# Kernel tuning notes

Measured on AMD Instinct MI355X. Metric: run time of the kernel, lower is better.

## Reference

```python
import jax, jax.numpy as jnp
import numpy as np

H, W = 496, 432  # ny, nx
C = 64           # pillar_dim == hidden_dim == NUM_BEV_FEATURES
B, N = 2, 8192   # batch size, non-empty pillars per batch
EPS = 1e-5


def _ln(x, g, b):
    m = jnp.mean(x, axis=-1, keepdims=True)
    v = jnp.var(x, axis=-1, keepdims=True)
    return (x - m) * jax.lax.rsqrt(v + EPS) * g + b


def _apply_rope(x):
    # x: [H, W, C] -> 2D RoPE-rotated features, matching torch reference math
    half = C // 2
    theta = 10000.0 ** (-(jnp.arange(half, dtype=jnp.float32) / half))
    h = jnp.linspace(-1.0, 1.0, H)
    w = jnp.linspace(-1.0, 1.0, W)
    hs = jnp.sin(h[:, None, None] * theta)  # [H,1,half]
    hc = jnp.cos(h[:, None, None] * theta)
    ws = jnp.sin(w[None, :, None] * theta)  # [1,W,half]
    wc = jnp.cos(w[None, :, None] * theta)
    x1, x2 = x[..., :half], x[..., half:]
    return jnp.concatenate(
        [x1 * hc * wc - x2 * hs * ws, x1 * hs * ws + x2 * hc * wc], axis=-1)


def setup_inputs() -> dict:
    key = jax.random.key(0)
    ks = jax.random.split(key, 8)
    rng = np.random.default_rng(0)
    # sorted UNIQUE flat indices per batch (boolean-mask gather order == sorted index order)
    idx = np.stack([np.sort(rng.choice(H * W, size=N, replace=False)) for _ in range(B)])
    s = 0.05
    return {
        "pillar_features": jax.random.normal(ks[0], (B, N, C), jnp.float32),
        "voxel_indices": jnp.asarray(idx, jnp.int32),
        "q_w": jax.random.normal(ks[1], (C, C), jnp.float32) * s,
        "q_b": jnp.zeros((C,), jnp.float32),
        "k_w": jax.random.normal(ks[2], (C, C), jnp.float32) * s,
        "k_b": jnp.zeros((C,), jnp.float32),
        "v_w": jax.random.normal(ks[3], (C, C), jnp.float32) * s,
        "v_b": jnp.zeros((C,), jnp.float32),
        "ffn_w1": jax.random.normal(ks[4], (C, C), jnp.float32) * s,
        "ffn_b1": jnp.zeros((C,), jnp.float32),
        "ffn_w2": jax.random.normal(ks[5], (C, C), jnp.float32) * s,
        "ffn_b2": jnp.zeros((C,), jnp.float32),
        "n1_g": jnp.ones((C,), jnp.float32),
        "n1_b": jnp.zeros((C,), jnp.float32),
        "n2_g": jnp.ones((C,), jnp.float32),
        "n2_b": jnp.zeros((C,), jnp.float32),
    }


def reference(pillar_features, voxel_indices, q_w, q_b, k_w, k_b, v_w, v_b,
              ffn_w1, ffn_b1, ffn_w2, ffn_b2, n1_g, n1_b, n2_g, n2_b):
    def per_batch(pillars, idx):
        # scatter pillars to dense BEV grid [H*W, C]
        dense = jnp.zeros((H * W, C), pillars.dtype).at[idx].set(pillars)
        x = dense.reshape(H, W, C)
        x = x + _apply_rope(x)                  # residual RoPE add
        flat = x.reshape(H * W, C)
        g = flat[idx]                           # masked gather (sorted index order)
        gn = _ln(g, n1_g, n1_b)
        Q = gn @ q_w.T + q_b                    # [N, C]
        K = gn @ k_w.T + k_b
        V = gn @ v_w.T + v_b
        attn = jax.nn.softmax(Q @ K.T, axis=-1)  # [N, N] full attention
        att = attn @ V + g
        h1 = jax.nn.gelu(_ln(att, n2_g, n2_b) @ ffn_w1.T + ffn_b1, approximate=False)
        upd = h1 @ ffn_w2.T + ffn_b2 + att
        out = flat.at[idx].set(upd)             # scatter back
        return out.T.reshape(C, H, W)
    return jax.vmap(per_batch)(pillar_features, voxel_indices)  # [B, C, H, W]
```

## Files before the change

### kernel.cpp

```cpp
#include <hip/hip_runtime.h>
#include <hip/hip_bf16.h>
#include <math.h>

#define HH 496
#define WW 432
#define CC 64
#define BB 2
#define NN 8192
#define HW_ (HH * WW)
#define SPLIT 8
#define KVPS (NN / SPLIT)
#define LOG2E 1.44269504088896f
#define DEFER_THR 11.541560327f

#if __has_builtin(__builtin_amdgcn_exp2f)
#define EXP2(x) __builtin_amdgcn_exp2f(x)
#else
#define EXP2(x) exp2f(x)
#endif

typedef __attribute__((ext_vector_type(8))) short bhalf8;
typedef __attribute__((ext_vector_type(4))) float f32x4;

__device__ __forceinline__ unsigned short f2bf(float f) {
  union { float f; unsigned int u; } v; v.f = f;
  unsigned int r = (v.u + 0x7fffu + ((v.u >> 16) & 1u)) >> 16;
  return (unsigned short)r;
}

__device__ __forceinline__ float bf2f(unsigned short u) {
  union { unsigned int u; float f; } v;
  v.u = ((unsigned int)u) << 16;
  return v.f;
}

__device__ __forceinline__ void gload16(const void* g, void* l) {
  __builtin_amdgcn_global_load_lds(
      (const __attribute__((address_space(1))) void*)g,
      (__attribute__((address_space(3))) void*)l, 16, 0, 0);
}

__global__ void prep_kernel(float* __restrict__ tabHS, float* __restrict__ tabHC,
                            float* __restrict__ tabWS, float* __restrict__ tabWC,
                            int* __restrict__ map) {
  int tid = blockIdx.x * blockDim.x + threadIdx.x;
  const int ntab = (HH + WW) * 32;
  if (tid < ntab) {
    int j = tid & 31;
    float theta = __expf(-(float)j * (9.210340371976184f / 32.f));
    if (tid < HH * 32) {
      int i = tid >> 5;
      float h = -1.f + 2.f * (float)i / (float)(HH - 1);
      float a = h * theta;
      tabHS[tid] = sinf(a);
      tabHC[tid] = cosf(a);
    } else {
      int t2 = tid - HH * 32;
      int i = t2 >> 5;
      float w = -1.f + 2.f * (float)i / (float)(WW - 1);
      float a = w * theta;
      tabWS[t2] = sinf(a);
      tabWC[t2] = cosf(a);
    }
  } else if (tid < ntab + BB * HW_) {
    map[tid - ntab] = -1;
  }
}

__global__ __launch_bounds__(256) void qkv_kernel(
    const float* __restrict__ pillar, const int* __restrict__ vidx,
    const float* __restrict__ tabHS, const float* __restrict__ tabHC,
    const float* __restrict__ tabWS, const float* __restrict__ tabWC,
    const float* __restrict__ qw, const float* __restrict__ kw,
    const float* __restrict__ vw,
    const float* __restrict__ qb, const float* __restrict__ kbias,
    const float* __restrict__ vb,
    const float* __restrict__ n1g, const float* __restrict__ n1b,
    float* __restrict__ g_out, unsigned short* __restrict__ Qb,
    unsigned short* __restrict__ Kb, unsigned short* __restrict__ Vt,
    int* __restrict__ map) {
  __shared__ unsigned short Aln[32][72];
  __shared__ unsigned short Wq[64][72], Wk[64][72], Wv[64][72];
  __shared__ unsigned int Vbo[64][20];
  int tid = threadIdx.x, wid = tid >> 6, lane = tid & 63;
  int l16 = lane & 15, lg = lane >> 4;
  int pt0 = blockIdx.x * 32;
  int b = pt0 >> 13, n0 = pt0 & (NN - 1);

  {
    int c = tid >> 2, k0 = (tid & 3) * 16;
#pragma unroll
    for (int mmm = 0; mmm < 3; mmm++) {
      const float* src = (mmm == 0 ? qw : mmm == 1 ? kw : vw) + c * 64 + k0;
      unsigned int pk[8];
#pragma unroll
      for (int j = 0; j < 8; j++) {
        float lo = src[2 * j], hi = src[2 * j + 1];
        asm("v_cvt_pk_bf16_f32 %0, %1, %2" : "=v"(pk[j]) : "v"(lo), "v"(hi));
      }
      unsigned short(*Wm)[72] = mmm == 0 ? Wq : mmm == 1 ? Wk : Wv;
      unsigned int* dst = (unsigned int*)&Wm[c][k0];
      *(uint4*)dst = make_uint4(pk[0], pk[1], pk[2], pk[3]);
      *(uint4*)(dst + 4) = make_uint4(pk[4], pk[5], pk[6], pk[7]);
    }
  }

  float n1g_l = n1g[lane], n1b_l = n1b[lane];
#pragma unroll 4
  for (int i = 0; i < 8; i++) {
    int p = wid * 8 + i;
    int pt = pt0 + p;
    float x = pillar[(size_t)pt * CC + lane];
    int pos = vidx[pt];
    int h = pos / WW, w = pos - h * WW;
    int j = lane & 31;
    float x1 = __shfl(x, j), x2 = __shfl(x, j + 32);
    float hs = tabHS[h * 32 + j], hc = tabHC[h * 32 + j];
    float ws = tabWS[w * 32 + j], wc = tabWC[w * 32 + j];
    float rope = (lane < 32) ? (x1 * hc * wc - x2 * hs * ws)
                             : (x1 * hs * ws + x2 * hc * wc);
    float gv = x + rope;
    g_out[(size_t)pt * CC + lane] = gv;
    float s = gv;
    for (int mm2 = 1; mm2 <= 32; mm2 <<= 1) s += __shfl_xor(s, mm2);
    float mean = s * (1.f / 64.f);
    float d = gv - mean;
    float vsum = d * d;
    for (int mm2 = 1; mm2 <= 32; mm2 <<= 1) vsum += __shfl_xor(vsum, mm2);
    float rstd = rsqrtf(vsum * (1.f / 64.f) + 1e-5f);
    float gn = d * rstd * n1g_l + n1b_l;
    Aln[p][lane] = f2bf(gn);
    if (lane == 0) map[b * HW_ + pos] = pt & (NN - 1);
  }
  __syncthreads();

#pragma unroll
  for (int j = 0; j < 6; j++) {
    int job = wid * 6 + j;
    int t = job / 12;
    int rem = job % 12;
    int mat = rem >> 2;
    int ct = rem & 3;
    bhalf8 aG0 = *(bhalf8*)&Aln[t * 16 + l16][lg * 8];
    bhalf8 aG1 = *(bhalf8*)&Aln[t * 16 + l16][32 + lg * 8];
    unsigned short(*Wm)[72] = mat == 0 ? Wq : mat == 1 ? Wk : Wv;
    bhalf8 bw0 = *(bhalf8*)&Wm[ct * 16 + l16][lg * 8];
    bhalf8 bw1 = *(bhalf8*)&Wm[ct * 16 + l16][32 + lg * 8];
    const float* bptr = mat == 0 ? qb : mat == 1 ? kbias : vb;
    float bias = bptr[ct * 16 + l16];
    f32x4 d = (f32x4){0.f, 0.f, 0.f, 0.f};
    d = __builtin_amdgcn_mfma_f32_16x16x32_bf16(aG0, bw0, d, 0, 0, 0);
    d = __builtin_amdgcn_mfma_f32_16x16x32_bf16(aG1, bw1, d, 0, 0, 0);
    if (mat == 0) {
#pragma unroll
      for (int r = 0; r < 4; r++) {
        size_t gi = (size_t)(pt0 + t * 16 + 4 * lg + r) * CC + ct * 16 + l16;
        Qb[gi] = f2bf((d[r] + bias) * LOG2E);
      }
    } else if (mat == 1) {
#pragma unroll
      for (int r = 0; r < 4; r++) {
        size_t gi = (size_t)(pt0 + t * 16 + 4 * lg + r) * CC + ct * 16 + l16;
        Kb[gi] = f2bf(d[r] + bias);
      }
    } else {
      float e0 = d[0] + bias, e1 = d[1] + bias;
      float e2 = d[2] + bias, e3 = d[3] + bias;
      unsigned int v0, v1;
      asm("v_cvt_pk_bf16_f32 %0, %1, %2" : "=v"(v0) : "v"(e0), "v"(e1));
      asm("v_cvt_pk_bf16_f32 %0, %1, %2" : "=v"(v1) : "v"(e2), "v"(e3));
      Vbo[ct * 16 + l16][t * 8 + 2 * lg + 0] = v0;
      Vbo[ct * 16 + l16][t * 8 + 2 * lg + 1] = v1;
    }
  }
  __syncthreads();
  {
    int c = tid >> 2, ch = tid & 3;
    uint4 w0 = *(uint4*)&Vbo[c][ch * 4];
    *(uint4*)(Vt + ((size_t)b * CC + c) * NN + n0 + ch * 8) = w0;
  }
}

__global__ __attribute__((amdgpu_flat_work_group_size(512, 512),
                          amdgpu_waves_per_eu(4, 4))) void attn_kernel(
    const unsigned short* __restrict__ Qb, const unsigned short* __restrict__ Kb,
    const unsigned short* __restrict__ Vt,
    unsigned short* __restrict__ OPb, float* __restrict__ Mb,
    float* __restrict__ Lb) {
  __shared__ unsigned short Kt[2][64 * 64];
  __shared__ unsigned short Vl[2][64 * 64];
  __shared__ unsigned short Plds[8][32][72];
  int tidx = threadIdx.x;
  int wid = tidx >> 6, lane = tidx & 63;
  int l16 = lane & 15, lg = lane >> 4;
  int blk = blockIdx.x;
  int s = blk & (SPLIT - 1);
  int tb = blk >> 3;
  int b = tb >> 5;
  int tile = tb & 31;
  int q0 = tile * 256 + wid * 32;
  int kvbeg = s * KVPS;
  const unsigned short* Q = Qb + (size_t)b * NN * CC;
  const unsigned short* K = Kb + (size_t)b * NN * CC;
  const unsigned short* V = Vt + (size_t)b * CC * NN;

  bhalf8 bQ0 = *(const bhalf8*)(Q + (size_t)(q0 + l16) * CC + lg * 8);
  bhalf8 bQ1 = *(const bhalf8*)(Q + (size_t)(q0 + l16) * CC + 32 + lg * 8);
  bhalf8 bQ2 = *(const bhalf8*)(Q + (size_t)(q0 + 16 + l16) * CC + lg * 8);
  bhalf8 bQ3 = *(const bhalf8*)(Q + (size_t)(q0 + 16 + l16) * CC + 32 + lg * 8);

  int r8 = lane >> 3, chn = lane & 7;
  int sch = chn ^ r8;
  const unsigned short* Ksrc = K + (size_t)(8 * wid + r8) * CC + sch * 8;
  const unsigned short* Vsrc = V + (size_t)(8 * wid + r8) * NN + sch * 8;
  unsigned short* KtW = &Kt[0][0] + (8 * wid) * 64;
  unsigned short* VlW = &Vl[0][0] + (8 * wid) * 64;

  f32x4 acc0[4], acc1[4];
#pragma unroll
  for (int i = 0; i < 4; i++) {
    acc0[i] = (f32x4){0.f, 0.f, 0.f, 0.f};
    acc1[i] = (f32x4){0.f, 0.f, 0.f, 0.f};
  }
  float m = -1e30f, Lp0 = 0.f, Lp1 = 0.f;
  int sw8 = (l16 & 7) * 8;

  auto stage = [&](int bufi, int kv0) {
    gload16(Ksrc + (size_t)kv0 * CC, KtW + bufi * 4096);
    gload16(Vsrc + kv0, VlW + bufi * 4096);
  };

  auto body = [&](int buf, int kv0) {
    const unsigned short* Kb_ = &Kt[buf][0];
    const unsigned short* Vb_ = &Vl[buf][0];
    f32x4 St[4], Su[4];
    __builtin_amdgcn_s_setprio(1);
#pragma unroll
    for (int t = 0; t < 4; t++) {
      const unsigned short* kr = Kb_ + (16 * t + l16) * 64;
      bhalf8 aK0 = *(const bhalf8*)(kr + ((lg * 8) ^ sw8));
      bhalf8 aK1 = *(const bhalf8*)(kr + (((lg + 4) * 8) ^ sw8));
      f32x4 sa = (f32x4){0.f, 0.f, 0.f, 0.f};
      f32x4 sb = (f32x4){0.f, 0.f, 0.f, 0.f};
      sa = __builtin_amdgcn_mfma_f32_16x16x32_bf16(aK0, bQ0, sa, 0, 0, 0);
      sa = __builtin_amdgcn_mfma_f32_16x16x32_bf16(aK1, bQ1, sa, 0, 0, 0);
      sb = __builtin_amdgcn_mfma_f32_16x16x32_bf16(aK0, bQ2, sb, 0, 0, 0);
      sb = __builtin_amdgcn_mfma_f32_16x16x32_bf16(aK1, bQ3, sb, 0, 0, 0);
      St[t] = sa;
      Su[t] = sb;
    }
    __builtin_amdgcn_s_setprio(0);
    float m0a = fmaxf(fmaxf(St[0][0], St[0][1]), fmaxf(St[0][2], St[0][3]));
    float m0b = fmaxf(fmaxf(St[1][0], St[1][1]), fmaxf(St[1][2], St[1][3]));
    float m0c = fmaxf(fmaxf(St[2][0], St[2][1]), fmaxf(St[2][2], St[2][3]));
    float m0d = fmaxf(fmaxf(St[3][0], St[3][1]), fmaxf(St[3][2], St[3][3]));
    float m1a = fmaxf(fmaxf(Su[0][0], Su[0][1]), fmaxf(Su[0][2], Su[0][3]));
    float m1b = fmaxf(fmaxf(Su[1][0], Su[1][1]), fmaxf(Su[1][2], Su[1][3]));
    float m1c = fmaxf(fmaxf(Su[2][0], Su[2][1]), fmaxf(Su[2][2], Su[2][3]));
    float m1d = fmaxf(fmaxf(Su[3][0], Su[3][1]), fmaxf(Su[3][2], Su[3][3]));
    float pm = fmaxf(fmaxf(fmaxf(m0a, m0b), fmaxf(m0c, m0d)),
                     fmaxf(fmaxf(m1a, m1b), fmaxf(m1c, m1d)));
    pm = fmaxf(pm, __shfl_xor(pm, 16));
    pm = fmaxf(pm, __shfl_xor(pm, 32));
    if (!__all(pm <= m + DEFER_THR)) {
      float mn = fmaxf(m, pm);
      float sc = EXP2(m - mn);
      m = mn;
      float scq[4];
#pragma unroll
      for (int r = 0; r < 4; r++) scq[r] = __shfl(sc, 4 * lg + r);
#pragma unroll
      for (int cg = 0; cg < 4; cg++)
#pragma unroll
        for (int r = 0; r < 4; r++) {
          acc0[cg][r] *= scq[r];
          acc1[cg][r] *= scq[r];
        }
      Lp0 *= sc;
      Lp1 *= sc;
    }
#pragma unroll
    for (int t = 0; t < 4; t++)
#pragma unroll
      for (int r = 0; r < 4; r++) {
        float p0 = EXP2(St[t][r] - m);
        float p1 = EXP2(Su[t][r] - m);
        St[t][r] = p0; Su[t][r] = p1;
        Lp0 += p0; Lp1 += p1;
      }
#pragma unroll
    for (int t = 0; t < 4; t++) {
      unsigned int pw0, pw1, pw2, pw3;
      float a0 = St[t][0], a1 = St[t][1], a2 = St[t][2], a3 = St[t][3];
      float b0 = Su[t][0], b1 = Su[t][1], b2 = Su[t][2], b3 = Su[t][3];
      asm("v_cvt_pk_bf16_f32 %0, %1, %2" : "=v"(pw0) : "v"(a0), "v"(a1));
      asm("v_cvt_pk_bf16_f32 %0, %1, %2" : "=v"(pw1) : "v"(a2), "v"(a3));
      asm("v_cvt_pk_bf16_f32 %0, %1, %2" : "=v"(pw2) : "v"(b0), "v"(b1));
      asm("v_cvt_pk_bf16_f32 %0, %1, %2" : "=v"(pw3) : "v"(b2), "v"(b3));
      *(uint2*)&Plds[wid][l16][16 * t + 4 * lg] = make_uint2(pw0, pw1);
      *(uint2*)&Plds[wid][16 + l16][16 * t + 4 * lg] = make_uint2(pw2, pw3);
    }
#pragma unroll
    for (int ch = 0; ch < 2; ch++) {
      bhalf8 aP0 = *(bhalf8*)&Plds[wid][l16][ch * 32 + lg * 8];
      bhalf8 aP1 = *(bhalf8*)&Plds[wid][16 + l16][ch * 32 + lg * 8];
      __builtin_amdgcn_s_setprio(1);
#pragma unroll
      for (int cg = 0; cg < 4; cg++) {
        bhalf8 bV = *(const bhalf8*)(Vb_ + (cg * 16 + l16) * 64 +
                                     (((4 * ch + lg) * 8) ^ sw8));
        acc0[cg] = __builtin_amdgcn_mfma_f32_16x16x32_bf16(aP0, bV, acc0[cg], 0, 0, 0);
        acc1[cg] = __builtin_amdgcn_mfma_f32_16x16x32_bf16(aP1, bV, acc1[cg], 0, 0, 0);
      }
      __builtin_amdgcn_s_setprio(0);
    }
  };

  stage(0, kvbeg);
  __syncthreads();
  const int nstep = KVPS / 64;
  for (int stp = 0; stp < nstep; stp += 2) {
    int kv0 = kvbeg + stp * 64;
    if (stp + 1 < nstep) stage(1, kv0 + 64);
    body(0, kv0);
    __syncthreads();
    if (stp + 2 < nstep) stage(0, kv0 + 128);
    body(1, kv0 + 64);
    __syncthreads();
  }
  size_t rowb = ((size_t)s * BB + b) * NN;
#pragma unroll
  for (int cg = 0; cg < 4; cg++)
#pragma unroll
    for (int r = 0; r < 4; r++) {
      OPb[(rowb + q0 + 4 * lg + r) * CC + cg * 16 + l16] = f2bf(acc0[cg][r]);
      OPb[(rowb + q0 + 16 + 4 * lg + r) * CC + cg * 16 + l16] = f2bf(acc1[cg][r]);
    }
  Lp0 += __shfl_xor(Lp0, 16);
  Lp0 += __shfl_xor(Lp0, 32);
  Lp1 += __shfl_xor(Lp1, 16);
  Lp1 += __shfl_xor(Lp1, 32);
  if (lg == 0) {
    Mb[rowb + q0 + l16] = m;
    Lb[rowb + q0 + l16] = Lp0;
    Mb[rowb + q0 + 16 + l16] = m;
    Lb[rowb + q0 + 16 + l16] = Lp1;
  }
}

__global__ __launch_bounds__(256) void ffn_kernel(
    const unsigned short* __restrict__ OPb, const float* __restrict__ Mb,
    const float* __restrict__ Lb, const float* __restrict__ g_in,
    const float* __restrict__ w1, const float* __restrict__ w2,
    const float* __restrict__ b1, const float* __restrict__ b2,
    const float* __restrict__ n2g, const float* __restrict__ n2b,
    float* __restrict__ upd) {
  __shared__ unsigned short Atile[32][72];
  __shared__ unsigned short Htile[32][72];
  __shared__ float aT[32][66];
  __shared__ unsigned short W1[64][72], W2[64][72];
  int tid = threadIdx.x, wid = tid >> 6, lane = tid & 63;
  int l16 = lane & 15, lg = lane >> 4;
  int pt0 = blockIdx.x * 32;

  {
    int c = tid >> 2, k0 = (tid & 3) * 16;
#pragma unroll
    for (int mmm = 0; mmm < 2; mmm++) {
      const float* src = (mmm == 0 ? w1 : w2) + c * 64 + k0;
      unsigned int pk[8];
#pragma unroll
      for (int j = 0; j < 8; j++) {
        float lo = src[2 * j], hi = src[2 * j + 1];
        asm("v_cvt_pk_bf16_f32 %0, %1, %2" : "=v"(pk[j]) : "v"(lo), "v"(hi));
      }
      unsigned short(*Wm)[72] = mmm == 0 ? W1 : W2;
      unsigned int* dst = (unsigned int*)&Wm[c][k0];
      *(uint4*)dst = make_uint4(pk[0], pk[1], pk[2], pk[3]);
      *(uint4*)(dst + 4) = make_uint4(pk[4], pk[5], pk[6], pk[7]);
    }
  }

  float n2g_l = n2g[lane], n2b_l = n2b[lane];
#pragma unroll 2
  for (int i = 0; i < 8; i++) {
    int p = wid * 8 + i;
    int pt = pt0 + p;
    float mv[SPLIT];
    float M = -1e30f;
#pragma unroll
    for (int s = 0; s < SPLIT; s++) {
      mv[s] = Mb[s * (BB * NN) + pt];
      M = fmaxf(M, mv[s]);
    }
    float accv = 0.f, Ls = 0.f;
#pragma unroll
    for (int s = 0; s < SPLIT; s++) {
      float w = EXP2(mv[s] - M);
      accv += w * bf2f(OPb[((size_t)s * (BB * NN) + pt) * CC + lane]);
      Ls += w * Lb[s * (BB * NN) + pt];
    }
    float a = accv / Ls + g_in[(size_t)pt * CC + lane];
    aT[p][lane] = a;
    float s2 = a;
    for (int mm2 = 1; mm2 <= 32; mm2 <<= 1) s2 += __shfl_xor(s2, mm2);
    float mean = s2 * (1.f / 64.f);
    float d = a - mean;
    float vsum = d * d;
    for (int mm2 = 1; mm2 <= 32; mm2 <<= 1) vsum += __shfl_xor(vsum, mm2);
    float rstd = rsqrtf(vsum * (1.f / 64.f) + 1e-5f);
    Atile[p][lane] = f2bf(d * rstd * n2g_l + n2b_l);
  }
  __syncthreads();

#pragma unroll
  for (int j = 0; j < 2; j++) {
    int job = wid * 2 + j;
    int t = job >> 2, ct = job & 3;
    bhalf8 aH0 = *(bhalf8*)&Atile[t * 16 + l16][lg * 8];
    bhalf8 aH1 = *(bhalf8*)&Atile[t * 16 + l16][32 + lg * 8];
    bhalf8 bw0 = *(bhalf8*)&W1[ct * 16 + l16][lg * 8];
    bhalf8 bw1 = *(bhalf8*)&W1[ct * 16 + l16][32 + lg * 8];
    float b1v = b1[ct * 16 + l16];
    f32x4 d1 = (f32x4){0.f, 0.f, 0.f, 0.f};
    d1 = __builtin_amdgcn_mfma_f32_16x16x32_bf16(aH0, bw0, d1, 0, 0, 0);
    d1 = __builtin_amdgcn_mfma_f32_16x16x32_bf16(aH1, bw1, d1, 0, 0, 0);
#pragma unroll
    for (int r = 0; r < 4; r++) {
      float h = d1[r] + b1v;
      h = 0.5f * h * (1.f + erff(h * 0.70710678118654752f));
      Htile[t * 16 + 4 * lg + r][ct * 16 + l16] = f2bf(h);
    }
  }
  __syncthreads();

#pragma unroll
  for (int j = 0; j < 2; j++) {
    int job = wid * 2 + j;
    int t = job >> 2, ct = job & 3;
    bhalf8 aF0 = *(bhalf8*)&Htile[t * 16 + l16][lg * 8];
    bhalf8 aF1 = *(bhalf8*)&Htile[t * 16 + l16][32 + lg * 8];
    bhalf8 bw0 = *(bhalf8*)&W2[ct * 16 + l16][lg * 8];
    bhalf8 bw1 = *(bhalf8*)&W2[ct * 16 + l16][32 + lg * 8];
    float b2v = b2[ct * 16 + l16];
    f32x4 d2 = (f32x4){0.f, 0.f, 0.f, 0.f};
    d2 = __builtin_amdgcn_mfma_f32_16x16x32_bf16(aF0, bw0, d2, 0, 0, 0);
    d2 = __builtin_amdgcn_mfma_f32_16x16x32_bf16(aF1, bw1, d2, 0, 0, 0);
#pragma unroll
    for (int r = 0; r < 4; r++) {
      int p = t * 16 + 4 * lg + r;
      upd[(size_t)(pt0 + p) * CC + ct * 16 + l16] = d2[r] + b2v + aT[p][ct * 16 + l16];
    }
  }
}

__global__ __launch_bounds__(256) void out_kernel(
    const int* __restrict__ map, const float* __restrict__ upd,
    float* __restrict__ out) {
  int b = blockIdx.x / (HW_ / 256);
  int pos = (blockIdx.x % (HW_ / 256)) * 256 + threadIdx.x;
  int r = map[b * HW_ + pos];
  float4 vals[16];
  if (r >= 0) {
    const float4* up = (const float4*)(upd + ((size_t)b * NN + r) * CC);
#pragma unroll
    for (int i = 0; i < 16; i++) vals[i] = up[i];
  } else {
#pragma unroll
    for (int i = 0; i < 16; i++) vals[i] = make_float4(0.f, 0.f, 0.f, 0.f);
  }
  float* o = out + (size_t)b * CC * HW_ + pos;
#pragma unroll
  for (int i = 0; i < 16; i++) {
    o[(size_t)(4 * i + 0) * HW_] = vals[i].x;
    o[(size_t)(4 * i + 1) * HW_] = vals[i].y;
    o[(size_t)(4 * i + 2) * HW_] = vals[i].z;
    o[(size_t)(4 * i + 3) * HW_] = vals[i].w;
  }
}

extern "C" void kernel_launch(void* const* d_in, const int* in_sizes, int n_in,
                              void* d_out, int out_size, void* d_ws, size_t ws_size,
                              hipStream_t stream) {
  const float* pillar = (const float*)d_in[0];
  const int* vidx = (const int*)d_in[1];
  const float* qw = (const float*)d_in[2];
  const float* qb = (const float*)d_in[3];
  const float* kw = (const float*)d_in[4];
  const float* kb = (const float*)d_in[5];
  const float* vw = (const float*)d_in[6];
  const float* vb = (const float*)d_in[7];
  const float* w1 = (const float*)d_in[8];
  const float* b1 = (const float*)d_in[9];
  const float* w2 = (const float*)d_in[10];
  const float* b2 = (const float*)d_in[11];
  const float* n1g = (const float*)d_in[12];
  const float* n1b = (const float*)d_in[13];
  const float* n2g = (const float*)d_in[14];
  const float* n2b = (const float*)d_in[15];
  float* out = (float*)d_out;

  char* ws = (char*)d_ws;
  size_t off = 0;
  auto take = [&](size_t bytes) -> char* {
    off = (off + 255) & ~(size_t)255;
    char* p = ws + off;
    off += bytes;
    return p;
  };
  float* tabHS = (float*)take((size_t)HH * 32 * 4);
  float* tabHC = (float*)take((size_t)HH * 32 * 4);
  float* tabWS = (float*)take((size_t)WW * 32 * 4);
  float* tabWC = (float*)take((size_t)WW * 32 * 4);
  float* gbuf = (float*)take((size_t)BB * NN * CC * 4);
  float* updb = (float*)take((size_t)BB * NN * CC * 4);
  unsigned short* Qb = (unsigned short*)take((size_t)BB * NN * CC * 2);
  unsigned short* Kb = (unsigned short*)take((size_t)BB * NN * CC * 2);
  unsigned short* Vt = (unsigned short*)take((size_t)BB * CC * NN * 2);
  unsigned short* OPb = (unsigned short*)take((size_t)SPLIT * BB * NN * CC * 2);
  float* Mbuf = (float*)take((size_t)SPLIT * BB * NN * 4);
  float* Lbuf = (float*)take((size_t)SPLIT * BB * NN * 4);
  int* map = (int*)take((size_t)BB * HW_ * 4);

  int preptot = (HH + WW) * 32 + BB * HW_;
  prep_kernel<<<(preptot + 255) / 256, 256, 0, stream>>>(
      tabHS, tabHC, tabWS, tabWC, map);
  qkv_kernel<<<BB * NN / 32, 256, 0, stream>>>(
      pillar, vidx, tabHS, tabHC, tabWS, tabWC, qw, kw, vw, qb, kb, vb,
      n1g, n1b, gbuf, Qb, Kb, Vt, map);
  attn_kernel<<<BB * (NN / 256) * SPLIT, 512, 0, stream>>>(Qb, Kb, Vt, OPb, Mbuf, Lbuf);
  ffn_kernel<<<BB * NN / 32, 256, 0, stream>>>(OPb, Mbuf, Lbuf, gbuf, w1, w2,
                                               b1, b2, n2g, n2b, updb);
  out_kernel<<<BB * (HW_ / 256), 256, 0, stream>>>(map, updb, out);
}
```

Measured before the change: 99.39 us.

## Double KV split, process query halves sequentially to cut registers, raise occupancy

The attention kernel's KV split count goes from 8 to 16, doubling the number of blocks and halving each block's KV range. The per-step body is split into two sequential half passes, one per 16-row query group, each with its own running max. This shrinks live score registers and the P staging buffer so the occupancy hint can rise from 4 to 6 waves per EU. The cost is more partial outputs for the FFN kernel to merge, more partial-output memory traffic, and repeated K/V LDS reads across the two halves.

```diff
diff --git a/kernel.cpp b/kernel.cpp
--- a/kernel.cpp
+++ b/kernel.cpp
@@ -8,7 +8,7 @@
 #define BB 2
 #define NN 8192
 #define HW_ (HH * WW)
-#define SPLIT 8
+#define SPLIT 16
 #define KVPS (NN / SPLIT)
 #define LOG2E 1.44269504088896f
 #define DEFER_THR 11.541560327f
@@ -182,20 +182,20 @@
 }
 
 __global__ __attribute__((amdgpu_flat_work_group_size(512, 512),
-                          amdgpu_waves_per_eu(4, 4))) void attn_kernel(
+                          amdgpu_waves_per_eu(6, 6))) void attn_kernel(
     const unsigned short* __restrict__ Qb, const unsigned short* __restrict__ Kb,
     const unsigned short* __restrict__ Vt,
     unsigned short* __restrict__ OPb, float* __restrict__ Mb,
     float* __restrict__ Lb) {
   __shared__ unsigned short Kt[2][64 * 64];
   __shared__ unsigned short Vl[2][64 * 64];
-  __shared__ unsigned short Plds[8][32][72];
+  __shared__ unsigned short Plds[8][16][72];
   int tidx = threadIdx.x;
   int wid = tidx >> 6, lane = tidx & 63;
   int l16 = lane & 15, lg = lane >> 4;
   int blk = blockIdx.x;
   int s = blk & (SPLIT - 1);
-  int tb = blk >> 3;
+  int tb = blk >> 4;
   int b = tb >> 5;
   int tile = tb & 31;
   int q0 = tile * 256 + wid * 32;
@@ -222,7 +222,7 @@
     acc0[i] = (f32x4){0.f, 0.f, 0.f, 0.f};
     acc1[i] = (f32x4){0.f, 0.f, 0.f, 0.f};
   }
-  float m = -1e30f, Lp0 = 0.f, Lp1 = 0.f;
+  float m0 = -1e30f, m1 = -1e30f, Lp0 = 0.f, Lp1 = 0.f;
   int sw8 = (l16 & 7) * 8;
 
   auto stage = [&](int bufi, int kv0) {
@@ -230,10 +230,10 @@
     gload16(Vsrc + kv0, VlW + bufi * 4096);
   };
 
-  auto body = [&](int buf, int kv0) {
-    const unsigned short* Kb_ = &Kt[buf][0];
-    const unsigned short* Vb_ = &Vl[buf][0];
-    f32x4 St[4], Su[4];
+  auto half_body = [&](const unsigned short* Kb_, const unsigned short* Vb_,
+                       bhalf8 bQa, bhalf8 bQb, float& mh, float& Lph,
+                       f32x4* acc) {
+    f32x4 St[4];
     __builtin_amdgcn_s_setprio(1);
 #pragma unroll
     for (int t = 0; t < 4; t++) {
@@ -241,79 +241,66 @@
       bhalf8 aK0 = *(const bhalf8*)(kr + ((lg * 8) ^ sw8));
       bhalf8 aK1 = *(const bhalf8*)(kr + (((lg + 4) * 8) ^ sw8));
       f32x4 sa = (f32x4){0.f, 0.f, 0.f, 0.f};
-      f32x4 sb = (f32x4){0.f, 0.f, 0.f, 0.f};
-      sa = __builtin_amdgcn_mfma_f32_16x16x32_bf16(aK0, bQ0, sa, 0, 0, 0);
-      sa = __builtin_amdgcn_mfma_f32_16x16x32_bf16(aK1, bQ1, sa, 0, 0, 0);
-      sb = __builtin_amdgcn_mfma_f32_16x16x32_bf16(aK0, bQ2, sb, 0, 0, 0);
-      sb = __builtin_amdgcn_mfma_f32_16x16x32_bf16(aK1, bQ3, sb, 0, 0, 0);
+      sa = __builtin_amdgcn_mfma_f32_16x16x32_bf16(aK0, bQa, sa, 0, 0, 0);
+      sa = __builtin_amdgcn_mfma_f32_16x16x32_bf16(aK1, bQb, sa, 0, 0, 0);
       St[t] = sa;
-      Su[t] = sb;
     }
     __builtin_amdgcn_s_setprio(0);
-    float m0a = fmaxf(fmaxf(St[0][0], St[0][1]), fmaxf(St[0][2], St[0][3]));
-    float m0b = fmaxf(fmaxf(St[1][0], St[1][1]), fmaxf(St[1][2], St[1][3]));
-    float m0c = fmaxf(fmaxf(St[2][0], St[2][1]), fmaxf(St[2][2], St[2][3]));
-    float m0d = fmaxf(fmaxf(St[3][0], St[3][1]), fmaxf(St[3][2], St[3][3]));
-    float m1a = fmaxf(fmaxf(Su[0][0], Su[0][1]), fmaxf(Su[0][2], Su[0][3]));
-    float m1b = fmaxf(fmaxf(Su[1][0], Su[1][1]), fmaxf(Su[1][2], Su[1][3]));
-    float m1c = fmaxf(fmaxf(Su[2][0], Su[2][1]), fmaxf(Su[2][2], Su[2][3]));
-    float m1d = fmaxf(fmaxf(Su[3][0], Su[3][1]), fmaxf(Su[3][2], Su[3][3]));
-    float pm = fmaxf(fmaxf(fmaxf(m0a, m0b), fmaxf(m0c, m0d)),
-                     fmaxf(fmaxf(m1a, m1b), fmaxf(m1c, m1d)));
+    float ma = fmaxf(fmaxf(St[0][0], St[0][1]), fmaxf(St[0][2], St[0][3]));
+    float mb = fmaxf(fmaxf(St[1][0], St[1][1]), fmaxf(St[1][2], St[1][3]));
+    float mc = fmaxf(fmaxf(St[2][0], St[2][1]), fmaxf(St[2][2], St[2][3]));
+    float md = fmaxf(fmaxf(St[3][0], St[3][1]), fmaxf(St[3][2], St[3][3]));
+    float pm = fmaxf(fmaxf(ma, mb), fmaxf(mc, md));
     pm = fmaxf(pm, __shfl_xor(pm, 16));
     pm = fmaxf(pm, __shfl_xor(pm, 32));
-    if (!__all(pm <= m + DEFER_THR)) {
-      float mn = fmaxf(m, pm);
-      float sc = EXP2(m - mn);
-      m = mn;
+    if (!__all(pm <= mh + DEFER_THR)) {
+      float mn = fmaxf(mh, pm);
+      float sc = EXP2(mh - mn);
+      mh = mn;
       float scq[4];
 #pragma unroll
       for (int r = 0; r < 4; r++) scq[r] = __shfl(sc, 4 * lg + r);
 #pragma unroll
       for (int cg = 0; cg < 4; cg++)
 #pragma unroll
-        for (int r = 0; r < 4; r++) {
-          acc0[cg][r] *= scq[r];
-          acc1[cg][r] *= scq[r];
-        }
-      Lp0 *= sc;
-      Lp1 *= sc;
+        for (int r = 0; r < 4; r++) acc[cg][r] *= scq[r];
+      Lph *= sc;
     }
 #pragma unroll
     for (int t = 0; t < 4; t++)
 #pragma unroll
       for (int r = 0; r < 4; r++) {
-        float p0 = EXP2(St[t][r] - m);
-        float p1 = EXP2(Su[t][r] - m);
-        St[t][r] = p0; Su[t][r] = p1;
-        Lp0 += p0; Lp1 += p1;
+        float p0 = EXP2(St[t][r] - mh);
+        St[t][r] = p0;
+        Lph += p0;
       }
 #pragma unroll
     for (int t = 0; t < 4; t++) {
-      unsigned int pw0, pw1, pw2, pw3;
+      unsigned int pw0, pw1;
       float a0 = St[t][0], a1 = St[t][1], a2 = St[t][2], a3 = St[t][3];
-      float b0 = Su[t][0], b1 = Su[t][1], b2 = Su[t][2], b3 = Su[t][3];
       asm("v_cvt_pk_bf16_f32 %0, %1, %2" : "=v"(pw0) : "v"(a0), "v"(a1));
       asm("v_cvt_pk_bf16_f32 %0, %1, %2" : "=v"(pw1) : "v"(a2), "v"(a3));
-      asm("v_cvt_pk_bf16_f32 %0, %1, %2" : "=v"(pw2) : "v"(b0), "v"(b1));
-      asm("v_cvt_pk_bf16_f32 %0, %1, %2" : "=v"(pw3) : "v"(b2), "v"(b3));
       *(uint2*)&Plds[wid][l16][16 * t + 4 * lg] = make_uint2(pw0, pw1);
-      *(uint2*)&Plds[wid][16 + l16][16 * t + 4 * lg] = make_uint2(pw2, pw3);
     }
 #pragma unroll
     for (int ch = 0; ch < 2; ch++) {
-      bhalf8 aP0 = *(bhalf8*)&Plds[wid][l16][ch * 32 + lg * 8];
-      bhalf8 aP1 = *(bhalf8*)&Plds[wid][16 + l16][ch * 32 + lg * 8];
+      bhalf8 aP = *(bhalf8*)&Plds[wid][l16][ch * 32 + lg * 8];
       __builtin_amdgcn_s_setprio(1);
 #pragma unroll
       for (int cg = 0; cg < 4; cg++) {
         bhalf8 bV = *(const bhalf8*)(Vb_ + (cg * 16 + l16) * 64 +
                                      (((4 * ch + lg) * 8) ^ sw8));
-        acc0[cg] = __builtin_amdgcn_mfma_f32_16x16x32_bf16(aP0, bV, acc0[cg], 0, 0, 0);
-        acc1[cg] = __builtin_amdgcn_mfma_f32_16x16x32_bf16(aP1, bV, acc1[cg], 0, 0, 0);
+        acc[cg] = __builtin_amdgcn_mfma_f32_16x16x32_bf16(aP, bV, acc[cg], 0, 0, 0);
       }
       __builtin_amdgcn_s_setprio(0);
     }
+  };
+
+  auto body = [&](int buf, int kv0) {
+    const unsigned short* Kb_ = &Kt[buf][0];
+    const unsigned short* Vb_ = &Vl[buf][0];
+    half_body(Kb_, Vb_, bQ0, bQ1, m0, Lp0, acc0);
+    half_body(Kb_, Vb_, bQ2, bQ3, m1, Lp1, acc1);
   };
 
   stage(0, kvbeg);
@@ -341,9 +328,9 @@
   Lp1 += __shfl_xor(Lp1, 16);
   Lp1 += __shfl_xor(Lp1, 32);
   if (lg == 0) {
-    Mb[rowb + q0 + l16] = m;
+    Mb[rowb + q0 + l16] = m0;
     Lb[rowb + q0 + l16] = Lp0;
-    Mb[rowb + q0 + 16 + l16] = m;
+    Mb[rowb + q0 + 16 + l16] = m1;
     Lb[rowb + q0 + 16 + l16] = Lp1;
   }
 }
@@ -386,8 +373,8 @@
   for (int i = 0; i < 8; i++) {
     int p = wid * 8 + i;
     int pt = pt0 + p;
+    float M = -1e30f;
     float mv[SPLIT];
-    float M = -1e30f;
 #pragma unroll
     for (int s = 0; s < SPLIT; s++) {
       mv[s] = Mb[s * (BB * NN) + pt];
```

New measurement: 257.1 us. 2.59x slower.

## Double KV split count and drop LDS double buffering in attention

Applied to the files above, without the earlier changes.

Raises the flash-decoding split factor from 8 to 16, doubling the attention grid while halving the KV range per block. The K/V LDS staging drops from two buffers to one, using a load, barrier, compute, barrier loop, and the waves-per-EU cap is relaxed. This targets a partly filled GPU, but it loses load/compute overlap, adds a barrier per step, and doubles the partial-output traffic and the combine work in the FFN kernel.

```diff
diff --git a/kernel.cpp b/kernel.cpp
--- a/kernel.cpp
+++ b/kernel.cpp
@@ -8,7 +8,7 @@
 #define BB 2
 #define NN 8192
 #define HW_ (HH * WW)
-#define SPLIT 8
+#define SPLIT 16
 #define KVPS (NN / SPLIT)
 #define LOG2E 1.44269504088896f
 #define DEFER_THR 11.541560327f
@@ -182,20 +182,20 @@
 }
 
 __global__ __attribute__((amdgpu_flat_work_group_size(512, 512),
-                          amdgpu_waves_per_eu(4, 4))) void attn_kernel(
+                          amdgpu_waves_per_eu(4))) void attn_kernel(
     const unsigned short* __restrict__ Qb, const unsigned short* __restrict__ Kb,
     const unsigned short* __restrict__ Vt,
     unsigned short* __restrict__ OPb, float* __restrict__ Mb,
     float* __restrict__ Lb) {
-  __shared__ unsigned short Kt[2][64 * 64];
-  __shared__ unsigned short Vl[2][64 * 64];
+  __shared__ unsigned short Kt[64 * 64];
+  __shared__ unsigned short Vl[64 * 64];
   __shared__ unsigned short Plds[8][32][72];
   int tidx = threadIdx.x;
   int wid = tidx >> 6, lane = tidx & 63;
   int l16 = lane & 15, lg = lane >> 4;
   int blk = blockIdx.x;
   int s = blk & (SPLIT - 1);
-  int tb = blk >> 3;
+  int tb = blk >> 4;
   int b = tb >> 5;
   int tile = tb & 31;
   int q0 = tile * 256 + wid * 32;
@@ -213,8 +213,8 @@
   int sch = chn ^ r8;
   const unsigned short* Ksrc = K + (size_t)(8 * wid + r8) * CC + sch * 8;
   const unsigned short* Vsrc = V + (size_t)(8 * wid + r8) * NN + sch * 8;
-  unsigned short* KtW = &Kt[0][0] + (8 * wid) * 64;
-  unsigned short* VlW = &Vl[0][0] + (8 * wid) * 64;
+  unsigned short* KtW = &Kt[0] + (8 * wid) * 64;
+  unsigned short* VlW = &Vl[0] + (8 * wid) * 64;
 
   f32x4 acc0[4], acc1[4];
 #pragma unroll
@@ -225,14 +225,14 @@
   float m = -1e30f, Lp0 = 0.f, Lp1 = 0.f;
   int sw8 = (l16 & 7) * 8;
 
-  auto stage = [&](int bufi, int kv0) {
-    gload16(Ksrc + (size_t)kv0 * CC, KtW + bufi * 4096);
-    gload16(Vsrc + kv0, VlW + bufi * 4096);
+  auto stage = [&](int kv0) {
+    gload16(Ksrc + (size_t)kv0 * CC, KtW);
+    gload16(Vsrc + kv0, VlW);
   };
 
-  auto body = [&](int buf, int kv0) {
-    const unsigned short* Kb_ = &Kt[buf][0];
-    const unsigned short* Vb_ = &Vl[buf][0];
+  auto body = [&]() {
+    const unsigned short* Kb_ = &Kt[0];
+    const unsigned short* Vb_ = &Vl[0];
     f32x4 St[4], Su[4];
     __builtin_amdgcn_s_setprio(1);
 #pragma unroll
@@ -316,16 +316,11 @@
     }
   };
 
-  stage(0, kvbeg);
-  __syncthreads();
   const int nstep = KVPS / 64;
-  for (int stp = 0; stp < nstep; stp += 2) {
-    int kv0 = kvbeg + stp * 64;
-    if (stp + 1 < nstep) stage(1, kv0 + 64);
-    body(0, kv0);
+  for (int stp = 0; stp < nstep; stp++) {
+    stage(kvbeg + stp * 64);
     __syncthreads();
-    if (stp + 2 < nstep) stage(0, kv0 + 128);
-    body(1, kv0 + 64);
+    body();
     __syncthreads();
   }
   size_t rowb = ((size_t)s * BB + b) * NN;
@@ -386,8 +381,8 @@
   for (int i = 0; i < 8; i++) {
     int p = wid * 8 + i;
     int pt = pt0 + p;
+    float M = -1e30f;
     float mv[SPLIT];
-    float M = -1e30f;
 #pragma unroll
     for (int s = 0; s < SPLIT; s++) {
       mv[s] = Mb[s * (BB * NN) + pt];
```

After: 104.6 us. 1.05x slower.
